# Performance work log

Hardware: AMD Instinct MI355X
Metric: run time of the kernel (lower is better)

## Reference

```python
import jax, jax.numpy as jnp
import numpy as np

N_NODES = 100000
N_EDGES = 1600000
IN_DIM = 128
HEADS = 8
HEAD_DIM = 16  # output_dim 128 / heads 8
NEG_SLOPE = 0.2  # PyG GATConv default LeakyReLU slope


def setup_inputs() -> dict:
    key = jax.random.key(0)
    k1, k2, k3, k4, k5 = jax.random.split(key, 5)
    x = jax.random.normal(k1, (N_NODES, IN_DIM), dtype=jnp.float32)
    edge_index = jax.random.randint(k2, (2, N_EDGES), 0, N_NODES, dtype=jnp.int64)
    scale = 1.0 / np.sqrt(IN_DIM)
    W = jax.random.normal(k3, (IN_DIM, HEADS * HEAD_DIM), dtype=jnp.float32) * scale
    a_src = jax.random.normal(k4, (HEADS, HEAD_DIM), dtype=jnp.float32) * scale
    a_dst = jax.random.normal(k5, (HEADS, HEAD_DIM), dtype=jnp.float32) * scale
    bias = jnp.zeros((HEADS * HEAD_DIM,), dtype=jnp.float32)
    return {"x": x, "edge_index": edge_index, "W": W, "a_src": a_src, "a_dst": a_dst, "bias": bias}


def reference(x, edge_index, W, a_src, a_dst, bias):
    N = x.shape[0]
    H, D = a_src.shape
    # add self-loops (PyG GATConv default add_self_loops=True)
    loop = jnp.arange(N, dtype=edge_index.dtype)
    src = jnp.concatenate([edge_index[0], loop])  # message sources j
    dst = jnp.concatenate([edge_index[1], loop])  # message targets i

    h = (x @ W).reshape(N, H, D)  # per-head projected features
    alpha_src = jnp.sum(h * a_src, axis=-1)  # [N, H]
    alpha_dst = jnp.sum(h * a_dst, axis=-1)  # [N, H]

    # edge-wise attention logits, softmax over incoming edges of each dst node
    e = jax.nn.leaky_relu(alpha_src[src] + alpha_dst[dst], NEG_SLOPE)  # [E', H]
    e_max = jax.ops.segment_max(e, dst, num_segments=N)
    e_exp = jnp.exp(e - e_max[dst])
    denom = jax.ops.segment_sum(e_exp, dst, num_segments=N)
    alpha = e_exp / (denom[dst] + 1e-16)  # [E', H]

    # weighted scatter-sum of source features
    out = jax.ops.segment_sum(alpha[:, :, None] * h[src], dst, num_segments=N)  # [N, H, D]
    out = out.reshape(N, H * D) + bias
    # wrapper: ReLU (concat=True), dropout is identity in eval mode
    return jax.nn.relu(out)
```

## Files before the change

kernel.cpp:

```cpp
#include <hip/hip_runtime.h>
#include <hip/hip_bf16.h>

#define NEG_SLOPE 0.2f
#define NBUCK 391
#define ABLK 8192
#define EPT 16

typedef __attribute__((ext_vector_type(8))) short bf16x8v;
typedef __attribute__((ext_vector_type(4))) float f32x4;

__device__ __forceinline__ unsigned f2bf_bits(float f) {
    unsigned u = __float_as_uint(f);
    return (u + 0x7fffu + ((u >> 16) & 1u)) >> 16;
}
__device__ __forceinline__ float bflo(unsigned u) { return __uint_as_float(u << 16); }
__device__ __forceinline__ float bfhi(unsigned u) { return __uint_as_float(u & 0xffff0000u); }

__global__ __launch_bounds__(256) void prep_w(const float* __restrict__ W,
                                              short* __restrict__ WtG) {
    int id = blockIdx.x * 256 + threadIdx.x;
    int n = id >> 7, k = id & 127;
    WtG[id] = (short)f2bf_bits(W[k * 128 + n]);
}

__global__ __launch_bounds__(256) void gemm_mfma(const float* __restrict__ x,
                                                 const short* __restrict__ WtG,
                                                 const float* __restrict__ a_src,
                                                 const float* __restrict__ a_dst,
                                                 short* __restrict__ hout,
                                                 float* __restrict__ as,
                                                 float* __restrict__ ad, int N) {
    __shared__ short xs[64 * 136];
    __shared__ short wt[128 * 136];
    const int tid = threadIdx.x;
    const int r0 = blockIdx.x * 64;

#pragma unroll
    for (int p = 0; p < 8; ++p) {
        int idx = p * 256 + tid;
        int n = idx >> 4, kk = (idx & 15) * 8;
        *(uint4*)&wt[n * 136 + kk] = *(const uint4*)(WtG + n * 128 + kk);
    }
#pragma unroll
    for (int p = 0; p < 8; ++p) {
        int lin = p * 1024 + tid * 4;
        int row = lin >> 7, k = lin & 127;
        int gr = r0 + row;
        int grc = gr < N ? gr : N - 1;
        float4 v = *(const float4*)(x + (size_t)grc * 128 + k);
        unsigned p0 = f2bf_bits(v.x) | (f2bf_bits(v.y) << 16);
        unsigned p1 = f2bf_bits(v.z) | (f2bf_bits(v.w) << 16);
        *(uint2*)&xs[row * 136 + k] = make_uint2(p0, p1);
    }
    __syncthreads();

    const int wv = tid >> 6;
    const int lane = tid & 63;
    const int lc = lane & 15, quad = lane >> 4;
    f32x4 acc[8];
#pragma unroll
    for (int c = 0; c < 8; ++c) acc[c] = (f32x4){0.f, 0.f, 0.f, 0.f};
    const short* aB = &xs[(wv * 16 + lc) * 136 + quad * 8];
    const short* bB = &wt[lc * 136 + quad * 8];
#pragma unroll
    for (int kc = 0; kc < 4; ++kc) {
        bf16x8v af = *(const bf16x8v*)(aB + kc * 32);
#pragma unroll
        for (int c = 0; c < 8; ++c) {
            bf16x8v bf = *(const bf16x8v*)(bB + c * (16 * 136) + kc * 32);
            acc[c] = __builtin_amdgcn_mfma_f32_16x16x32_bf16(af, bf, acc[c], 0, 0, 0);
        }
    }

    const int rowb = r0 + wv * 16 + quad * 4;
#pragma unroll
    for (int c = 0; c < 8; ++c) {
        float asc = a_src[c * 16 + lc];
        float adc = a_dst[c * 16 + lc];
        float sv[4], dv[4];
#pragma unroll
        for (int r = 0; r < 4; ++r) {
            float hv = acc[c][r];
            int row = rowb + r;
            if (row < N) hout[(size_t)row * 128 + c * 16 + lc] = (short)f2bf_bits(hv);
            sv[r] = hv * asc;
            dv[r] = hv * adc;
        }
#pragma unroll
        for (int m = 1; m <= 8; m <<= 1) {
#pragma unroll
            for (int r = 0; r < 4; ++r) {
                sv[r] += __shfl_xor(sv[r], m);
                dv[r] += __shfl_xor(dv[r], m);
            }
        }
        if (lc == 0) {
#pragma unroll
            for (int r = 0; r < 4; ++r) {
                int row = rowb + r;
                if (row < N) { as[row * 8 + c] = sv[r]; ad[row * 8 + c] = dv[r]; }
            }
        }
    }
}

__global__ __launch_bounds__(512) void bucket_edges(const int* __restrict__ ei, int E,
                                                    uint2* __restrict__ slab,
                                                    int* __restrict__ cntG,
                                                    int* __restrict__ startG) {
    __shared__ int sS[ABLK];
    __shared__ int dS[ABLK];
    __shared__ int hist[512];
    __shared__ int cur[NBUCK];
    const int t = threadIdx.x;
    const int blk = blockIdx.x;
    const int base = blk * ABLK;
    int count = E - base; if (count > ABLK) count = ABLK;

    hist[t] = 0;
#pragma unroll
    for (int k = 0; k < EPT; ++k) {
        int i = k * 512 + t;
        int idx = base + i;
        if (i < count) { sS[i] = ei[idx]; dS[i] = ei[E + idx]; }
    }
    __syncthreads();
#pragma unroll
    for (int k = 0; k < EPT; ++k) {
        int i = k * 512 + t;
        if (i < count) atomicAdd(&hist[dS[i] >> 8], 1);
    }
    __syncthreads();
    int v = hist[t];
    for (int off = 1; off < 512; off <<= 1) {
        int u = t >= off ? hist[t - off] : 0;
        __syncthreads();
        hist[t] += u;
        __syncthreads();
    }
    int excl = hist[t] - v;
    if (t < NBUCK) {
        cntG[blk * NBUCK + t]   = v;
        startG[blk * NBUCK + t] = excl;
        cur[t] = excl;
    }
    __syncthreads();
#pragma unroll
    for (int k = 0; k < EPT; ++k) {
        int i = k * 512 + t;
        if (i < count) {
            int d = dS[i];
            int pos = atomicAdd(&cur[d >> 8], 1);
            slab[(size_t)blk * ABLK + pos] = make_uint2((unsigned)sS[i], (unsigned)d);
        }
    }
}

__global__ __launch_bounds__(64) void bucket_totals(const int* __restrict__ cntG, int nblk,
                                                    int* __restrict__ totalG) {
    int b = blockIdx.x;
    int lane = threadIdx.x;
    int s = 0;
    for (int blk = lane; blk < nblk; blk += 64) s += cntG[blk * NBUCK + b];
#pragma unroll
    for (int off = 32; off > 0; off >>= 1) s += __shfl_down(s, off);
    if (lane == 0) totalG[b] = s;
}

__global__ __launch_bounds__(512) void scan_buckets(const int* __restrict__ totalG,
                                                    int* __restrict__ bucketStart) {
    __shared__ int s[512];
    int t = threadIdx.x;
    int v = t < NBUCK ? totalG[t] : 0;
    s[t] = v;
    __syncthreads();
    for (int off = 1; off < 512; off <<= 1) {
        int u = t >= off ? s[t - off] : 0;
        __syncthreads();
        s[t] += u;
        __syncthreads();
    }
    int excl = s[t] - v;
    if (t <= NBUCK) bucketStart[t] = excl;
}

__global__ __launch_bounds__(512) void build_csr(const uint2* __restrict__ slab,
                                                 const int* __restrict__ cntG,
                                                 const int* __restrict__ startG,
                                                 const int* __restrict__ bucketStart,
                                                 int nblk, int N, int E,
                                                 int* __restrict__ rowptr,
                                                 int* __restrict__ sortedSrc) {
    __shared__ uint2 eL[ABLK];
    __shared__ int incl[512];
    __shared__ int cS[512];
    __shared__ int stS[512];
    __shared__ int hist[512];
    __shared__ int lp[256];
    const int b = blockIdx.x;
    const int t = threadIdx.x;
    const int nodeBase = b << 8;

    int c = 0, st = 0;
    if (t < nblk) { c = cntG[t * NBUCK + b]; st = startG[t * NBUCK + b]; }
    cS[t] = c; stS[t] = st; hist[t] = 0; incl[t] = c;
    __syncthreads();
    for (int off = 1; off < 512; off <<= 1) {
        int u = t >= off ? incl[t - off] : 0;
        __syncthreads();
        incl[t] += u;
        __syncthreads();
    }
    const int total = incl[511];
    for (int e = t; e < total; e += 512) {
        int lo = 0, hi = 511;
        while (lo < hi) { int mid = (lo + hi) >> 1; if (incl[mid] > e) hi = mid; else lo = mid + 1; }
        int loc = e - (incl[lo] - cS[lo]);
        eL[e] = slab[(size_t)lo * ABLK + stS[lo] + loc];
    }
    __syncthreads();
    for (int e = t; e < total; e += 512) atomicAdd(&hist[eL[e].y & 255], 1);
    __syncthreads();
    int hv = hist[t];
    for (int off = 1; off < 512; off <<= 1) {
        int u = t >= off ? hist[t - off] : 0;
        __syncthreads();
        hist[t] += u;
        __syncthreads();
    }
    int hexcl = hist[t] - hv;
    const int bs = bucketStart[b];
    int nodes = N - nodeBase; if (nodes > 256) nodes = 256;
    if (t < nodes) rowptr[nodeBase + t] = bs + hexcl;
    if (t < 256) lp[t] = hexcl;
    if (b == gridDim.x - 1 && t == 0) rowptr[N] = E;
    __syncthreads();
    for (int e = t; e < total; e += 512) {
        uint2 ed = eL[e];
        int pos = atomicAdd(&lp[ed.y & 255], 1);
        sortedSrc[bs + pos] = (int)ed.x;
    }
}

__global__ __launch_bounds__(256) void aggregate(const int* __restrict__ rowptr,
                                                 const int* __restrict__ sortedSrc,
                                                 const short* __restrict__ h,
                                                 const float* __restrict__ as,
                                                 const float* __restrict__ ad,
                                                 const float* __restrict__ bias,
                                                 float* __restrict__ out, int N) {
    int node = blockIdx.x * 4 + (threadIdx.x >> 6);
    if (node >= N) return;
    int lane = threadIdx.x & 63;
    int g = lane >> 4, p = lane & 15, hh = p >> 1;
    int start = rowptr[node], end = rowptr[node + 1];
    float adv = ad[node * 8 + hh];

    float acc[8];
#pragma unroll
    for (int k = 0; k < 8; ++k) acc[k] = 0.f;
    float dsum = 0.f;

    int e = start + g;
    int j = (e < end) ? sortedSrc[e] : 0;
    while (e < end) {
        int jn = (e + 4 < end) ? sortedSrc[e + 4] : 0;
        float t = as[j * 8 + hh] + adv;
        t = t > 0.f ? t : NEG_SLOPE * t;
        float w = __expf(t);
        uint4 hv = *(const uint4*)(h + (size_t)j * 128 + p * 8);
        acc[0] += w * bflo(hv.x); acc[1] += w * bfhi(hv.x);
        acc[2] += w * bflo(hv.y); acc[3] += w * bfhi(hv.y);
        acc[4] += w * bflo(hv.z); acc[5] += w * bfhi(hv.z);
        acc[6] += w * bflo(hv.w); acc[7] += w * bfhi(hv.w);
        dsum += w;
        j = jn; e += 4;
    }
#pragma unroll
    for (int m = 16; m <= 32; m <<= 1) {
#pragma unroll
        for (int k = 0; k < 8; ++k) acc[k] += __shfl_xor(acc[k], m);
        dsum += __shfl_xor(dsum, m);
    }
    {
        float t = as[node * 8 + hh] + adv;
        t = t > 0.f ? t : NEG_SLOPE * t;
        float w = __expf(t);
        uint4 hv = *(const uint4*)(h + (size_t)node * 128 + p * 8);
        acc[0] += w * bflo(hv.x); acc[1] += w * bfhi(hv.x);
        acc[2] += w * bflo(hv.y); acc[3] += w * bfhi(hv.y);
        acc[4] += w * bflo(hv.z); acc[5] += w * bfhi(hv.z);
        acc[6] += w * bflo(hv.w); acc[7] += w * bfhi(hv.w);
        dsum += w;
    }
    float inv = 1.0f / (dsum + 1e-16f);
    float4 b0 = *(const float4*)(bias + p * 8);
    float4 b1 = *(const float4*)(bias + p * 8 + 4);
    float o0 = acc[0] * inv + b0.x, o1 = acc[1] * inv + b0.y;
    float o2 = acc[2] * inv + b0.z, o3 = acc[3] * inv + b0.w;
    float o4 = acc[4] * inv + b1.x, o5 = acc[5] * inv + b1.y;
    float o6 = acc[6] * inv + b1.z, o7 = acc[7] * inv + b1.w;
    o0 = o0 > 0.f ? o0 : 0.f; o1 = o1 > 0.f ? o1 : 0.f;
    o2 = o2 > 0.f ? o2 : 0.f; o3 = o3 > 0.f ? o3 : 0.f;
    o4 = o4 > 0.f ? o4 : 0.f; o5 = o5 > 0.f ? o5 : 0.f;
    o6 = o6 > 0.f ? o6 : 0.f; o7 = o7 > 0.f ? o7 : 0.f;
    *(float4*)(out + (size_t)node * 128 + p * 8)     = make_float4(o0, o1, o2, o3);
    *(float4*)(out + (size_t)node * 128 + p * 8 + 4) = make_float4(o4, o5, o6, o7);
}

extern "C" void kernel_launch(void* const* d_in, const int* in_sizes, int n_in,
                              void* d_out, int out_size, void* d_ws, size_t ws_size,
                              hipStream_t stream) {
    const float* x     = (const float*)d_in[0];
    const int*   ei    = (const int*)d_in[1];
    const float* W     = (const float*)d_in[2];
    const float* a_src = (const float*)d_in[3];
    const float* a_dst = (const float*)d_in[4];
    const float* bias  = (const float*)d_in[5];
    float* out = (float*)d_out;

    const int N = in_sizes[0] / 128;
    const int E = in_sizes[1] / 2;
    const int nblk = (E + ABLK - 1) / ABLK;

    char* ws = (char*)d_ws;
    size_t off = 0;
    auto alloc = [&](size_t bytes) { void* p = ws + off; off = (off + bytes + 255) & ~(size_t)255; return p; };
    short* h         = (short*)alloc((size_t)N * 128 * 2);
    float* as        = (float*)alloc((size_t)N * 8 * 4);
    float* ad        = (float*)alloc((size_t)N * 8 * 4);
    int*   sortedSrc = (int*)alloc((size_t)E * 4);
    int*   rowptr    = (int*)alloc((size_t)(N + 1) * 4);
    uint2* slab      = (uint2*)alloc((size_t)nblk * ABLK * 8);
    int*   cntG      = (int*)alloc((size_t)nblk * NBUCK * 4);
    int*   startG    = (int*)alloc((size_t)nblk * NBUCK * 4);
    int*   totalG    = (int*)alloc((size_t)NBUCK * 4);
    int*   bucketSt  = (int*)alloc((size_t)(NBUCK + 1) * 4);
    short* WtG       = (short*)alloc((size_t)128 * 128 * 2);

    bucket_edges<<<nblk, 512, 0, stream>>>(ei, E, slab, cntG, startG);
    bucket_totals<<<NBUCK, 64, 0, stream>>>(cntG, nblk, totalG);
    scan_buckets<<<1, 512, 0, stream>>>(totalG, bucketSt);
    build_csr<<<NBUCK, 512, 0, stream>>>(slab, cntG, startG, bucketSt, nblk, N, E, rowptr, sortedSrc);

    prep_w<<<64, 256, 0, stream>>>(W, WtG);
    gemm_mfma<<<(N + 63) / 64, 256, 0, stream>>>(x, WtG, a_src, a_dst, h, as, ad, N);

    aggregate<<<(N + 3) / 4, 256, 0, stream>>>(rowptr, sortedSrc, h, as, ad, bias, out, N);
}
```

Baseline: 255.5 us.

## Fuse CSR build into aggregation with per-bucket shared-memory edge sort

Edges are now bucketed into 128-node buckets with source and local destination packed into one 32-bit word. A single fused kernel gathers each bucket's edges into shared memory, counting-sorts them by local node and aggregates directly. This drops the global rowptr/sortedSrc arrays and the bucket_totals, scan_buckets and separate aggregate launches. The cost is fewer, larger blocks that each process 128 nodes with 8 waves, which reduces parallelism and load balance. A fixed shared capacity of 3072 edges per bucket could overflow on skewed degree distributions, and packing the source into 17 bits caps the node count at 131072.

```diff
diff --git a/kernel.cpp b/kernel.cpp
--- a/kernel.cpp
+++ b/kernel.cpp
@@ -2,9 +2,9 @@
 #include <hip/hip_bf16.h>
 
 #define NEG_SLOPE 0.2f
-#define NBUCK 391
+#define NBUCK 782
 #define ABLK 8192
-#define EPT 16
+#define CAP 3072
 
 typedef __attribute__((ext_vector_type(8))) short bf16x8v;
 typedef __attribute__((ext_vector_type(4))) float f32x4;
@@ -104,35 +104,33 @@
     }
 }
 
-__global__ __launch_bounds__(512) void bucket_edges(const int* __restrict__ ei, int E,
-                                                    uint2* __restrict__ slab,
-                                                    int* __restrict__ cntG,
-                                                    int* __restrict__ startG) {
-    __shared__ int sS[ABLK];
-    __shared__ int dS[ABLK];
-    __shared__ int hist[512];
+__global__ __launch_bounds__(1024) void bucket_edges(const int* __restrict__ ei, int E,
+                                                     unsigned* __restrict__ slab,
+                                                     int* __restrict__ cntG,
+                                                     int* __restrict__ startG) {
+    __shared__ int hist[1024];
     __shared__ int cur[NBUCK];
     const int t = threadIdx.x;
     const int blk = blockIdx.x;
     const int base = blk * ABLK;
     int count = E - base; if (count > ABLK) count = ABLK;
 
+    int sr[8], dr[8];
     hist[t] = 0;
 #pragma unroll
-    for (int k = 0; k < EPT; ++k) {
-        int i = k * 512 + t;
-        int idx = base + i;
-        if (i < count) { sS[i] = ei[idx]; dS[i] = ei[E + idx]; }
-    }
-    __syncthreads();
-#pragma unroll
-    for (int k = 0; k < EPT; ++k) {
-        int i = k * 512 + t;
-        if (i < count) atomicAdd(&hist[dS[i] >> 8], 1);
+    for (int k = 0; k < 8; ++k) {
+        int i = k * 1024 + t;
+        if (i < count) { sr[k] = ei[base + i]; dr[k] = ei[E + base + i]; }
+    }
+    __syncthreads();
+#pragma unroll
+    for (int k = 0; k < 8; ++k) {
+        int i = k * 1024 + t;
+        if (i < count) atomicAdd(&hist[dr[k] >> 7], 1);
     }
     __syncthreads();
     int v = hist[t];
-    for (int off = 1; off < 512; off <<= 1) {
+    for (int off = 1; off < 1024; off <<= 1) {
         int u = t >= off ? hist[t - off] : 0;
         __syncthreads();
         hist[t] += u;
@@ -146,64 +144,40 @@
     }
     __syncthreads();
 #pragma unroll
-    for (int k = 0; k < EPT; ++k) {
-        int i = k * 512 + t;
+    for (int k = 0; k < 8; ++k) {
+        int i = k * 1024 + t;
         if (i < count) {
-            int d = dS[i];
-            int pos = atomicAdd(&cur[d >> 8], 1);
-            slab[(size_t)blk * ABLK + pos] = make_uint2((unsigned)sS[i], (unsigned)d);
-        }
-    }
-}
-
-__global__ __launch_bounds__(64) void bucket_totals(const int* __restrict__ cntG, int nblk,
-                                                    int* __restrict__ totalG) {
-    int b = blockIdx.x;
-    int lane = threadIdx.x;
-    int s = 0;
-    for (int blk = lane; blk < nblk; blk += 64) s += cntG[blk * NBUCK + b];
-#pragma unroll
-    for (int off = 32; off > 0; off >>= 1) s += __shfl_down(s, off);
-    if (lane == 0) totalG[b] = s;
-}
-
-__global__ __launch_bounds__(512) void scan_buckets(const int* __restrict__ totalG,
-                                                    int* __restrict__ bucketStart) {
-    __shared__ int s[512];
-    int t = threadIdx.x;
-    int v = t < NBUCK ? totalG[t] : 0;
-    s[t] = v;
-    __syncthreads();
-    for (int off = 1; off < 512; off <<= 1) {
-        int u = t >= off ? s[t - off] : 0;
-        __syncthreads();
-        s[t] += u;
-        __syncthreads();
-    }
-    int excl = s[t] - v;
-    if (t <= NBUCK) bucketStart[t] = excl;
-}
-
-__global__ __launch_bounds__(512) void build_csr(const uint2* __restrict__ slab,
-                                                 const int* __restrict__ cntG,
-                                                 const int* __restrict__ startG,
-                                                 const int* __restrict__ bucketStart,
-                                                 int nblk, int N, int E,
-                                                 int* __restrict__ rowptr,
-                                                 int* __restrict__ sortedSrc) {
-    __shared__ uint2 eL[ABLK];
+            int d = dr[k];
+            int pos = atomicAdd(&cur[d >> 7], 1);
+            slab[(size_t)blk * ABLK + pos] = (unsigned)sr[k] | ((unsigned)(d & 127) << 17);
+        }
+    }
+}
+
+__global__ __launch_bounds__(512) void bucket_aggregate(const unsigned* __restrict__ slab,
+                                                        const int* __restrict__ cntG,
+                                                        const int* __restrict__ startG,
+                                                        int nblk, int N,
+                                                        const short* __restrict__ h,
+                                                        const float* __restrict__ as,
+                                                        const float* __restrict__ ad,
+                                                        const float* __restrict__ bias,
+                                                        float* __restrict__ out) {
+    __shared__ int eL[CAP];
+    __shared__ int sortedL[CAP];
     __shared__ int incl[512];
     __shared__ int cS[512];
     __shared__ int stS[512];
-    __shared__ int hist[512];
-    __shared__ int lp[256];
-    const int b = blockIdx.x;
+    __shared__ int rs[128];
+    __shared__ int lp[128];
+    const int bb = blockIdx.x;
     const int t = threadIdx.x;
-    const int nodeBase = b << 8;
+    const int nodeBase = bb << 7;
 
     int c = 0, st = 0;
-    if (t < nblk) { c = cntG[t * NBUCK + b]; st = startG[t * NBUCK + b]; }
-    cS[t] = c; stS[t] = st; hist[t] = 0; incl[t] = c;
+    if (t < nblk) { c = cntG[t * NBUCK + bb]; st = startG[t * NBUCK + bb]; }
+    cS[t] = c; stS[t] = st; incl[t] = c;
+    if (t < 128) lp[t] = 0;
     __syncthreads();
     for (int off = 1; off < 512; off <<= 1) {
         int u = t >= off ? incl[t - off] : 0;
@@ -213,99 +187,93 @@
     }
     const int total = incl[511];
     for (int e = t; e < total; e += 512) {
-        int lo = 0, hi = 511;
+        int lo = 0, hi = nblk - 1;
         while (lo < hi) { int mid = (lo + hi) >> 1; if (incl[mid] > e) hi = mid; else lo = mid + 1; }
         int loc = e - (incl[lo] - cS[lo]);
-        eL[e] = slab[(size_t)lo * ABLK + stS[lo] + loc];
-    }
-    __syncthreads();
-    for (int e = t; e < total; e += 512) atomicAdd(&hist[eL[e].y & 255], 1);
-    __syncthreads();
-    int hv = hist[t];
-    for (int off = 1; off < 512; off <<= 1) {
-        int u = t >= off ? hist[t - off] : 0;
-        __syncthreads();
-        hist[t] += u;
-        __syncthreads();
-    }
-    int hexcl = hist[t] - hv;
-    const int bs = bucketStart[b];
-    int nodes = N - nodeBase; if (nodes > 256) nodes = 256;
-    if (t < nodes) rowptr[nodeBase + t] = bs + hexcl;
-    if (t < 256) lp[t] = hexcl;
-    if (b == gridDim.x - 1 && t == 0) rowptr[N] = E;
+        eL[e] = (int)slab[(size_t)lo * ABLK + stS[lo] + loc];
+    }
+    __syncthreads();
+    for (int e = t; e < total; e += 512) atomicAdd(&lp[((unsigned)eL[e]) >> 17], 1);
+    __syncthreads();
+    int hv = (t < 128) ? lp[t] : 0;
+    for (int off = 1; off < 128; off <<= 1) {
+        int u = (t >= off && t < 128) ? lp[t - off] : 0;
+        __syncthreads();
+        if (t < 128) lp[t] += u;
+        __syncthreads();
+    }
+    if (t < 128) {
+        int ex = lp[t] - hv;
+        rs[t] = ex;
+        lp[t] = ex;
+    }
     __syncthreads();
     for (int e = t; e < total; e += 512) {
-        uint2 ed = eL[e];
-        int pos = atomicAdd(&lp[ed.y & 255], 1);
-        sortedSrc[bs + pos] = (int)ed.x;
-    }
-}
-
-__global__ __launch_bounds__(256) void aggregate(const int* __restrict__ rowptr,
-                                                 const int* __restrict__ sortedSrc,
-                                                 const short* __restrict__ h,
-                                                 const float* __restrict__ as,
-                                                 const float* __restrict__ ad,
-                                                 const float* __restrict__ bias,
-                                                 float* __restrict__ out, int N) {
-    int node = blockIdx.x * 4 + (threadIdx.x >> 6);
-    if (node >= N) return;
-    int lane = threadIdx.x & 63;
-    int g = lane >> 4, p = lane & 15, hh = p >> 1;
-    int start = rowptr[node], end = rowptr[node + 1];
-    float adv = ad[node * 8 + hh];
-
-    float acc[8];
-#pragma unroll
-    for (int k = 0; k < 8; ++k) acc[k] = 0.f;
-    float dsum = 0.f;
-
-    int e = start + g;
-    int j = (e < end) ? sortedSrc[e] : 0;
-    while (e < end) {
-        int jn = (e + 4 < end) ? sortedSrc[e + 4] : 0;
-        float t = as[j * 8 + hh] + adv;
-        t = t > 0.f ? t : NEG_SLOPE * t;
-        float w = __expf(t);
-        uint4 hv = *(const uint4*)(h + (size_t)j * 128 + p * 8);
-        acc[0] += w * bflo(hv.x); acc[1] += w * bfhi(hv.x);
-        acc[2] += w * bflo(hv.y); acc[3] += w * bfhi(hv.y);
-        acc[4] += w * bflo(hv.z); acc[5] += w * bfhi(hv.z);
-        acc[6] += w * bflo(hv.w); acc[7] += w * bfhi(hv.w);
-        dsum += w;
-        j = jn; e += 4;
-    }
-#pragma unroll
-    for (int m = 16; m <= 32; m <<= 1) {
-#pragma unroll
-        for (int k = 0; k < 8; ++k) acc[k] += __shfl_xor(acc[k], m);
-        dsum += __shfl_xor(dsum, m);
-    }
-    {
-        float t = as[node * 8 + hh] + adv;
-        t = t > 0.f ? t : NEG_SLOPE * t;
-        float w = __expf(t);
-        uint4 hv = *(const uint4*)(h + (size_t)node * 128 + p * 8);
-        acc[0] += w * bflo(hv.x); acc[1] += w * bfhi(hv.x);
-        acc[2] += w * bflo(hv.y); acc[3] += w * bfhi(hv.y);
-        acc[4] += w * bflo(hv.z); acc[5] += w * bfhi(hv.z);
-        acc[6] += w * bflo(hv.w); acc[7] += w * bfhi(hv.w);
-        dsum += w;
-    }
-    float inv = 1.0f / (dsum + 1e-16f);
+        unsigned pk = (unsigned)eL[e];
+        int pos = atomicAdd(&lp[pk >> 17], 1);
+        sortedL[pos] = (int)(pk & 0x1FFFFu);
+    }
+    __syncthreads();
+    const int wv = t >> 6;
+    const int lane = t & 63;
+    const int g = lane >> 4, p = lane & 15, hh = p >> 1;
     float4 b0 = *(const float4*)(bias + p * 8);
     float4 b1 = *(const float4*)(bias + p * 8 + 4);
-    float o0 = acc[0] * inv + b0.x, o1 = acc[1] * inv + b0.y;
-    float o2 = acc[2] * inv + b0.z, o3 = acc[3] * inv + b0.w;
-    float o4 = acc[4] * inv + b1.x, o5 = acc[5] * inv + b1.y;
-    float o6 = acc[6] * inv + b1.z, o7 = acc[7] * inv + b1.w;
-    o0 = o0 > 0.f ? o0 : 0.f; o1 = o1 > 0.f ? o1 : 0.f;
-    o2 = o2 > 0.f ? o2 : 0.f; o3 = o3 > 0.f ? o3 : 0.f;
-    o4 = o4 > 0.f ? o4 : 0.f; o5 = o5 > 0.f ? o5 : 0.f;
-    o6 = o6 > 0.f ? o6 : 0.f; o7 = o7 > 0.f ? o7 : 0.f;
-    *(float4*)(out + (size_t)node * 128 + p * 8)     = make_float4(o0, o1, o2, o3);
-    *(float4*)(out + (size_t)node * 128 + p * 8 + 4) = make_float4(o4, o5, o6, o7);
+    for (int nl = wv * 16; nl < wv * 16 + 16; ++nl) {
+        int gn = nodeBase + nl;
+        if (gn >= N) break;
+        int s0 = rs[nl], e0 = lp[nl];
+        float adv = ad[gn * 8 + hh];
+
+        float acc[8];
+#pragma unroll
+        for (int k = 0; k < 8; ++k) acc[k] = 0.f;
+        float dsum = 0.f;
+
+        int e = s0 + g;
+        int j = (e < e0) ? sortedL[e] : 0;
+        while (e < e0) {
+            int jn = (e + 4 < e0) ? sortedL[e + 4] : 0;
+            float tt = as[j * 8 + hh] + adv;
+            tt = tt > 0.f ? tt : NEG_SLOPE * tt;
+            float w = __expf(tt);
+            uint4 hr = *(const uint4*)(h + (size_t)j * 128 + p * 8);
+            acc[0] += w * bflo(hr.x); acc[1] += w * bfhi(hr.x);
+            acc[2] += w * bflo(hr.y); acc[3] += w * bfhi(hr.y);
+            acc[4] += w * bflo(hr.z); acc[5] += w * bfhi(hr.z);
+            acc[6] += w * bflo(hr.w); acc[7] += w * bfhi(hr.w);
+            dsum += w;
+            j = jn; e += 4;
+        }
+#pragma unroll
+        for (int m = 16; m <= 32; m <<= 1) {
+#pragma unroll
+            for (int k = 0; k < 8; ++k) acc[k] += __shfl_xor(acc[k], m);
+            dsum += __shfl_xor(dsum, m);
+        }
+        {
+            float tt = as[gn * 8 + hh] + adv;
+            tt = tt > 0.f ? tt : NEG_SLOPE * tt;
+            float w = __expf(tt);
+            uint4 hr = *(const uint4*)(h + (size_t)gn * 128 + p * 8);
+            acc[0] += w * bflo(hr.x); acc[1] += w * bfhi(hr.x);
+            acc[2] += w * bflo(hr.y); acc[3] += w * bfhi(hr.y);
+            acc[4] += w * bflo(hr.z); acc[5] += w * bfhi(hr.z);
+            acc[6] += w * bflo(hr.w); acc[7] += w * bfhi(hr.w);
+            dsum += w;
+        }
+        float inv = 1.0f / (dsum + 1e-16f);
+        float o0 = acc[0] * inv + b0.x, o1 = acc[1] * inv + b0.y;
+        float o2 = acc[2] * inv + b0.z, o3 = acc[3] * inv + b0.w;
+        float o4 = acc[4] * inv + b1.x, o5 = acc[5] * inv + b1.y;
+        float o6 = acc[6] * inv + b1.z, o7 = acc[7] * inv + b1.w;
+        o0 = o0 > 0.f ? o0 : 0.f; o1 = o1 > 0.f ? o1 : 0.f;
+        o2 = o2 > 0.f ? o2 : 0.f; o3 = o3 > 0.f ? o3 : 0.f;
+        o4 = o4 > 0.f ? o4 : 0.f; o5 = o5 > 0.f ? o5 : 0.f;
+        o6 = o6 > 0.f ? o6 : 0.f; o7 = o7 > 0.f ? o7 : 0.f;
+        *(float4*)(out + (size_t)gn * 128 + p * 8)     = make_float4(o0, o1, o2, o3);
+        *(float4*)(out + (size_t)gn * 128 + p * 8 + 4) = make_float4(o4, o5, o6, o7);
+    }
 }
 
 extern "C" void kernel_launch(void* const* d_in, const int* in_sizes, int n_in,
@@ -326,25 +294,17 @@
     char* ws = (char*)d_ws;
     size_t off = 0;
     auto alloc = [&](size_t bytes) { void* p = ws + off; off = (off + bytes + 255) & ~(size_t)255; return p; };
-    short* h         = (short*)alloc((size_t)N * 128 * 2);
-    float* as        = (float*)alloc((size_t)N * 8 * 4);
-    float* ad        = (float*)alloc((size_t)N * 8 * 4);
-    int*   sortedSrc = (int*)alloc((size_t)E * 4);
-    int*   rowptr    = (int*)alloc((size_t)(N + 1) * 4);
-    uint2* slab      = (uint2*)alloc((size_t)nblk * ABLK * 8);
-    int*   cntG      = (int*)alloc((size_t)nblk * NBUCK * 4);
-    int*   startG    = (int*)alloc((size_t)nblk * NBUCK * 4);
-    int*   totalG    = (int*)alloc((size_t)NBUCK * 4);
-    int*   bucketSt  = (int*)alloc((size_t)(NBUCK + 1) * 4);
-    short* WtG       = (short*)alloc((size_t)128 * 128 * 2);
-
-    bucket_edges<<<nblk, 512, 0, stream>>>(ei, E, slab, cntG, startG);
-    bucket_totals<<<NBUCK, 64, 0, stream>>>(cntG, nblk, totalG);
-    scan_buckets<<<1, 512, 0, stream>>>(totalG, bucketSt);
-    build_csr<<<NBUCK, 512, 0, stream>>>(slab, cntG, startG, bucketSt, nblk, N, E, rowptr, sortedSrc);
+    short*    h      = (short*)alloc((size_t)N * 128 * 2);
+    float*    as     = (float*)alloc((size_t)N * 8 * 4);
+    float*    ad     = (float*)alloc((size_t)N * 8 * 4);
+    unsigned* slab   = (unsigned*)alloc((size_t)nblk * ABLK * 4);
+    int*      cntG   = (int*)alloc((size_t)nblk * NBUCK * 4);
+    int*      startG = (int*)alloc((size_t)nblk * NBUCK * 4);
+    short*    WtG    = (short*)alloc((size_t)128 * 128 * 2);
 
     prep_w<<<64, 256, 0, stream>>>(W, WtG);
     gemm_mfma<<<(N + 63) / 64, 256, 0, stream>>>(x, WtG, a_src, a_dst, h, as, ad, N);
-
-    aggregate<<<(N + 3) / 4, 256, 0, stream>>>(rowptr, sortedSrc, h, as, ad, bias, out, N);
-}
+    bucket_edges<<<nblk, 1024, 0, stream>>>(ei, E, slab, cntG, startG);
+    bucket_aggregate<<<NBUCK, 512, 0, stream>>>(slab, cntG, startG, nblk, N,
+                                                h, as, ad, bias, out);
+}
```

Result: faster. 248.7 us (-2.7%).
